# Kernel tuning notes

Hardware: AMD Instinct MI355X
Metric: run time of the kernel (lower is better)

Reference implementation:

```python
import jax, jax.numpy as jnp
import numpy as np

EPS = 1e-08
CJS_WEIGHT = 0.5  # init kwarg `weight`
B, C = 4096, 8192


def setup_inputs() -> dict:
    key = jax.random.key(0)
    k1, k2 = jax.random.split(key)
    pred_logit = jax.random.normal(k1, (B, C), dtype=jnp.float32)
    gt_raw = jax.random.uniform(k2, (B, C), dtype=jnp.float32) + EPS
    gt = gt_raw / jnp.sum(gt_raw, axis=1, keepdims=True)  # row-stochastic target distribution
    return {"pred_logit": pred_logit, "gt": gt}


def reference(pred_logit, gt):
    xlogy = jax.scipy.special.xlogy
    n, c = pred_logit.shape

    # CrossEntropyLoss with soft (probability) targets, mean over batch
    logp = jax.nn.log_softmax(pred_logit, axis=1)
    ce = -jnp.mean(jnp.sum(gt * logp, axis=1))

    # CJS loss: sum_{i=1..C} 0.5*(KL(D_{:i} || m_{:i}) + KL(P_{:i} || m_{:i})) / B
    # Column j contributes to every prefix i > j, i.e. with weight (C - j):
    # one fused weighted-sum pass instead of the O(C^2) prefix loop.
    p = jnp.exp(logp)                      # softmax(pred_logit)
    m = 0.5 * (gt + p + EPS)
    logm = jnp.log(m)
    contrib = (xlogy(gt, gt) - gt * logm) + (xlogy(p, p) - p * logm)  # [B, C]
    w = (c - jnp.arange(c)).astype(pred_logit.dtype)                   # prefix multiplicity
    cjs = 0.5 * jnp.sum(contrib * w) / n   # 'batchmean' divides by B

    return ce + CJS_WEIGHT * cjs
```

## Files before the change

### kernel.cpp

```cpp
#include <hip/hip_runtime.h>

#define EPSF   1e-8f
#define NROWS  4096
#define NCOLS  8192
#define F4ROW  (NCOLS / 4)
#define K2_BLOCKS 2048
#define K2_TPB    256
#define NTHREADS  (K2_BLOCKS * K2_TPB)
#define ITERS     ((NROWS * F4ROW) / NTHREADS)
#define LOG2E  1.44269504088896340736f
#define LN2    0.693147180559945309417f

#if __has_builtin(__builtin_amdgcn_exp2f)
#define EXP2F(x) __builtin_amdgcn_exp2f(x)
#else
#define EXP2F(x) exp2f(x)
#endif
#if __has_builtin(__builtin_amdgcn_logf)
#define LOG2F(x) __builtin_amdgcn_logf(x)
#else
#define LOG2F(x) log2f(x)
#endif

__global__ __launch_bounds__(256) void k_rowsum(const float* __restrict__ pred,
                                                float* __restrict__ ls2) {
    __shared__ float sA[4];
    const int row = blockIdx.x, tid = threadIdx.x, lane = tid & 63, wid = tid >> 6;
    const float4* pr = (const float4*)(pred + (size_t)row * NCOLS);
    float s = 0.f;
    #pragma unroll
    for (int i = 0; i < 8; ++i) {
        float4 v = pr[tid + i * 256];
        s += (EXP2F(v.x * LOG2E) + EXP2F(v.y * LOG2E))
           + (EXP2F(v.z * LOG2E) + EXP2F(v.w * LOG2E));
    }
    #pragma unroll
    for (int off = 1; off < 64; off <<= 1) s += __shfl_xor(s, off, 64);
    if (lane == 0) sA[wid] = s;
    __syncthreads();
    if (tid == 0) ls2[row] = LOG2F(sA[0] + sA[1] + sA[2] + sA[3]);
}

__global__ __launch_bounds__(K2_TPB) void k_main(const float* __restrict__ pred,
                                                 const float* __restrict__ gt,
                                                 const float* __restrict__ ls2,
                                                 double2* __restrict__ partial) {
    __shared__ float sce[4], scj[4];
    const int tid0 = blockIdx.x * K2_TPB + threadIdx.x;
    const float4* pr = (const float4*)pred;
    const float4* gr = (const float4*)gt;

    float ce2 = 0.f, cj2 = 0.f;
    #pragma unroll 4
    for (int it = 0; it < ITERS; ++it) {
        const int f  = tid0 + it * NTHREADS;
        float4 v  = pr[f];
        float4 g4 = gr[f];
        float ls  = ls2[f >> 11];
        const float wbase = (float)(NCOLS - ((f & (F4ROW - 1)) << 2));
        #pragma unroll
        for (int k = 0; k < 4; ++k) {
            float x = (&v.x)[k], g = (&g4.x)[k];
            float lp2 = fmaf(x, LOG2E, -ls);
            float p   = EXP2F(lp2);
            ce2 = fmaf(g, lp2, ce2);
            float m   = fmaf(0.5f, g + p, 0.5f * EPSF);
            float l2m = LOG2F(m);
            float l2g = LOG2F(g);
            float contrib = g * (l2g - l2m) + p * (lp2 - l2m);
            cj2 = fmaf(contrib, wbase - (float)k, cj2);
        }
    }
    const int lane = threadIdx.x & 63, wid = threadIdx.x >> 6;
    #pragma unroll
    for (int off = 1; off < 64; off <<= 1) {
        ce2 += __shfl_xor(ce2, off, 64);
        cj2 += __shfl_xor(cj2, off, 64);
    }
    if (lane == 0) { sce[wid] = ce2; scj[wid] = cj2; }
    __syncthreads();
    if (threadIdx.x == 0) {
        double a = (double)sce[0] + (double)sce[1] + (double)sce[2] + (double)sce[3];
        double b = (double)scj[0] + (double)scj[1] + (double)scj[2] + (double)scj[3];
        partial[blockIdx.x] = make_double2(a, b);
    }
}

__global__ __launch_bounds__(1024) void k_final(const double2* __restrict__ partial,
                                                float* __restrict__ out) {
    __shared__ double sce[16], scj[16];
    const int tid = threadIdx.x, lane = tid & 63, wid = tid >> 6;
    double ce = 0.0, cj = 0.0;
    #pragma unroll
    for (int i = tid; i < K2_BLOCKS; i += 1024) {
        double2 d = partial[i];
        ce += d.x; cj += d.y;
    }
    #pragma unroll
    for (int off = 1; off < 64; off <<= 1) {
        ce += __shfl_xor(ce, off, 64);
        cj += __shfl_xor(cj, off, 64);
    }
    if (lane == 0) { sce[wid] = ce; scj[wid] = cj; }
    __syncthreads();
    if (tid == 0) {
        double a = 0.0, b = 0.0;
        #pragma unroll
        for (int i = 0; i < 16; ++i) { a += sce[i]; b += scj[i]; }
        out[0] = (float)(((-a + 0.25 * b) * (double)LN2) / (double)NROWS);
    }
}

extern "C" void kernel_launch(void* const* d_in, const int* in_sizes, int n_in,
                              void* d_out, int out_size, void* d_ws, size_t ws_size,
                              hipStream_t stream) {
    const float* pred = (const float*)d_in[0];
    const float* gt   = (const float*)d_in[1];
    float*   ls2     = (float*)d_ws;
    double2* partial = (double2*)((char*)d_ws + NROWS * sizeof(float));
    k_rowsum<<<NROWS, 256, 0, stream>>>(pred, ls2);
    k_main<<<K2_BLOCKS, K2_TPB, 0, stream>>>(pred, gt, ls2, partial);
    k_final<<<1, 1024, 0, stream>>>(partial, (float*)d_out);
}
```

Baseline: 278.0 us.

## Fuse row logsumexp and main loss pass into one row-per-block kernel

Merges the row-sum kernel and the main loss kernel into a single kernel where each 512-thread block owns one row. Each block keeps the pred row in registers across the logsumexp reduction and then reuses it for the loss pass. This removes the second global read of pred and one kernel launch. In exchange it needs more registers per thread and inserts a block barrier between the two phases, which can lower occupancy and latency hiding.

```diff
diff --git a/kernel.cpp b/kernel.cpp
--- a/kernel.cpp
+++ b/kernel.cpp
@@ -3,11 +3,7 @@
 #define EPSF   1e-8f
 #define NROWS  4096
 #define NCOLS  8192
-#define F4ROW  (NCOLS / 4)
-#define K2_BLOCKS 2048
-#define K2_TPB    256
-#define NTHREADS  (K2_BLOCKS * K2_TPB)
-#define ITERS     ((NROWS * F4ROW) / NTHREADS)
+#define TPB    512
 #define LOG2E  1.44269504088896340736f
 #define LN2    0.693147180559945309417f
 
@@ -22,45 +18,53 @@
 #define LOG2F(x) log2f(x)
 #endif
 
-__global__ __launch_bounds__(256) void k_rowsum(const float* __restrict__ pred,
-                                                float* __restrict__ ls2) {
-    __shared__ float sA[4];
-    const int row = blockIdx.x, tid = threadIdx.x, lane = tid & 63, wid = tid >> 6;
+__global__ __launch_bounds__(TPB) void cecjs_fused(const float* __restrict__ pred,
+                                                   const float* __restrict__ gt,
+                                                   double2* __restrict__ partial) {
+    __shared__ float  sA[8];
+    __shared__ double sce[8], scj[8];
+
+    const int row  = blockIdx.x;
+    const int tid  = threadIdx.x;
+    const int lane = tid & 63;
+    const int wid  = tid >> 6;
+
     const float4* pr = (const float4*)(pred + (size_t)row * NCOLS);
+    const float4* gr = (const float4*)(gt   + (size_t)row * NCOLS);
+
+    float4 v[4];
+    #pragma unroll
+    for (int i = 0; i < 4; ++i) v[i] = pr[tid + i * TPB];
     float s = 0.f;
     #pragma unroll
-    for (int i = 0; i < 8; ++i) {
-        float4 v = pr[tid + i * 256];
-        s += (EXP2F(v.x * LOG2E) + EXP2F(v.y * LOG2E))
-           + (EXP2F(v.z * LOG2E) + EXP2F(v.w * LOG2E));
-    }
+    for (int i = 0; i < 4; ++i)
+        s += (EXP2F(v[i].x * LOG2E) + EXP2F(v[i].y * LOG2E))
+           + (EXP2F(v[i].z * LOG2E) + EXP2F(v[i].w * LOG2E));
     #pragma unroll
     for (int off = 1; off < 64; off <<= 1) s += __shfl_xor(s, off, 64);
     if (lane == 0) sA[wid] = s;
+
+    #pragma unroll
+    for (int i = 0; i < 4; ++i)
+        asm volatile("" : "+v"(v[i].x), "+v"(v[i].y), "+v"(v[i].z), "+v"(v[i].w));
+
     __syncthreads();
-    if (tid == 0) ls2[row] = LOG2F(sA[0] + sA[1] + sA[2] + sA[3]);
-}
+    float tot = 0.f;
+    #pragma unroll
+    for (int i = 0; i < 8; ++i) tot += sA[i];
+    const float ls = LOG2F(tot);
 
-__global__ __launch_bounds__(K2_TPB) void k_main(const float* __restrict__ pred,
-                                                 const float* __restrict__ gt,
-                                                 const float* __restrict__ ls2,
-                                                 double2* __restrict__ partial) {
-    __shared__ float sce[4], scj[4];
-    const int tid0 = blockIdx.x * K2_TPB + threadIdx.x;
-    const float4* pr = (const float4*)pred;
-    const float4* gr = (const float4*)gt;
+    float4 g4[4];
+    #pragma unroll
+    for (int i = 0; i < 4; ++i) g4[i] = gr[tid + i * TPB];
 
     float ce2 = 0.f, cj2 = 0.f;
-    #pragma unroll 4
-    for (int it = 0; it < ITERS; ++it) {
-        const int f  = tid0 + it * NTHREADS;
-        float4 v  = pr[f];
-        float4 g4 = gr[f];
-        float ls  = ls2[f >> 11];
-        const float wbase = (float)(NCOLS - ((f & (F4ROW - 1)) << 2));
+    #pragma unroll
+    for (int i = 0; i < 4; ++i) {
+        const float wbase = (float)(NCOLS - (tid + i * TPB) * 4);
         #pragma unroll
         for (int k = 0; k < 4; ++k) {
-            float x = (&v.x)[k], g = (&g4.x)[k];
+            float x = (&v[i].x)[k], g = (&g4[i].x)[k];
             float lp2 = fmaf(x, LOG2E, -ls);
             float p   = EXP2F(lp2);
             ce2 = fmaf(g, lp2, ce2);
@@ -71,18 +75,18 @@
             cj2 = fmaf(contrib, wbase - (float)k, cj2);
         }
     }
-    const int lane = threadIdx.x & 63, wid = threadIdx.x >> 6;
     #pragma unroll
     for (int off = 1; off < 64; off <<= 1) {
         ce2 += __shfl_xor(ce2, off, 64);
         cj2 += __shfl_xor(cj2, off, 64);
     }
-    if (lane == 0) { sce[wid] = ce2; scj[wid] = cj2; }
+    if (lane == 0) { sce[wid] = (double)ce2; scj[wid] = (double)cj2; }
     __syncthreads();
-    if (threadIdx.x == 0) {
-        double a = (double)sce[0] + (double)sce[1] + (double)sce[2] + (double)sce[3];
-        double b = (double)scj[0] + (double)scj[1] + (double)scj[2] + (double)scj[3];
-        partial[blockIdx.x] = make_double2(a, b);
+    if (tid == 0) {
+        double a = 0.0, b = 0.0;
+        #pragma unroll
+        for (int i = 0; i < 8; ++i) { a += sce[i]; b += scj[i]; }
+        partial[row] = make_double2(a, b);
     }
 }
 
@@ -92,7 +96,7 @@
     const int tid = threadIdx.x, lane = tid & 63, wid = tid >> 6;
     double ce = 0.0, cj = 0.0;
     #pragma unroll
-    for (int i = tid; i < K2_BLOCKS; i += 1024) {
+    for (int i = tid; i < NROWS; i += 1024) {
         double2 d = partial[i];
         ce += d.x; cj += d.y;
     }
@@ -116,9 +120,7 @@
                               hipStream_t stream) {
     const float* pred = (const float*)d_in[0];
     const float* gt   = (const float*)d_in[1];
-    float*   ls2     = (float*)d_ws;
-    double2* partial = (double2*)((char*)d_ws + NROWS * sizeof(float));
-    k_rowsum<<<NROWS, 256, 0, stream>>>(pred, ls2);
-    k_main<<<K2_BLOCKS, K2_TPB, 0, stream>>>(pred, gt, ls2, partial);
+    double2* partial  = (double2*)d_ws;
+    cecjs_fused<<<NROWS, TPB, 0, stream>>>(pred, gt, partial);
     k_final<<<1, 1024, 0, stream>>>(partial, (float*)d_out);
 }
```

Measured after the change: 276.3 us. No clear change (-0.6%).
